# Kernel optimization log

Hardware: AMD Instinct MI355X
Metric: run time of the kernel (lower is better)

The kernel has to match this reference:

```python
import jax, jax.numpy as jnp
import numpy as np

HEADS = 8
DIM_HEAD = 64
QUERY_DIM = 512
CONTEXT_DIM = 768
INNER = HEADS * DIM_HEAD  # 512
SCALE = DIM_HEAD ** -0.5


def setup_inputs() -> dict:
    key = jax.random.key(0)
    ks = jax.random.split(key, 7)
    B, N, M = 4, 2048, 2048
    x = jax.random.normal(ks[0], (B, N, QUERY_DIM), dtype=jnp.float32)
    context = jax.random.normal(ks[1], (B, M, CONTEXT_DIM), dtype=jnp.float32)
    # torch Linear weights: [out_features, in_features], y = x @ W.T
    s = 0.02
    Wq = jax.random.normal(ks[2], (INNER, QUERY_DIM), dtype=jnp.float32) * s
    Wk = jax.random.normal(ks[3], (INNER, CONTEXT_DIM), dtype=jnp.float32) * s
    Wv = jax.random.normal(ks[4], (INNER, CONTEXT_DIM), dtype=jnp.float32) * s
    Wo = jax.random.normal(ks[5], (QUERY_DIM, INNER), dtype=jnp.float32) * s
    bo = jax.random.normal(ks[6], (QUERY_DIM,), dtype=jnp.float32) * s
    return {"x": x, "context": context, "Wq": Wq, "Wk": Wk, "Wv": Wv, "Wo": Wo, "bo": bo}


def reference(x, context, Wq, Wk, Wv, Wo, bo):
    b, n, _ = x.shape
    m = context.shape[1]
    h, d = HEADS, DIM_HEAD
    # Projections (bias=False for q/k/v)
    q = jnp.einsum('bnc,ec->bne', x, Wq)        # [b, n, inner]
    k = jnp.einsum('bmc,ec->bme', context, Wk)  # [b, m, inner]
    v = jnp.einsum('bmc,ec->bme', context, Wv)
    # Split heads
    q = q.reshape(b, n, h, d)
    k = k.reshape(b, m, h, d)
    v = v.reshape(b, m, h, d)
    # Scores in fp32 (original casts q,k to float), scaled by dim_head**-0.5
    sim = jnp.einsum('bihd,bjhd->bhij', q.astype(jnp.float32), k.astype(jnp.float32)) * SCALE
    attn = jax.nn.softmax(sim, axis=-1).astype(v.dtype)
    out = jnp.einsum('bhij,bjhd->bihd', attn, v).reshape(b, n, h * d)
    # Output projection with bias (dropout=0 -> identity)
    return jnp.einsum('bne,oe->bno', out, Wo) + bo
```

## Files before the change

### kernel.cpp

```cpp
#include <hip/hip_runtime.h>
#include <hip/hip_bf16.h>
#include <math.h>


typedef __bf16 bf16x8 __attribute__((ext_vector_type(8)));
typedef __bf16 bf16x4 __attribute__((ext_vector_type(4)));
typedef float f32x4 __attribute__((ext_vector_type(4)));

#define QSCALE 0.18033688011112042f

#if __has_builtin(__builtin_amdgcn_exp2f)
#define EXP2(x) __builtin_amdgcn_exp2f(x)
#else
#define EXP2(x) exp2f(x)
#endif

__device__ __forceinline__ f32x4 mfma32(bf16x8 a, bf16x8 b, f32x4 c) {
  return __builtin_amdgcn_mfma_f32_16x16x32_bf16(a, b, c, 0, 0, 0);
}

__global__ __launch_bounds__(256) void cast_all(
    const float* __restrict__ x, const float* __restrict__ ctx,
    const float* __restrict__ wq, const float* __restrict__ wk,
    const float* __restrict__ wv, const float* __restrict__ wo,
    __bf16* __restrict__ xb, __bf16* __restrict__ cb,
    __bf16* __restrict__ wqb, __bf16* __restrict__ wkb,
    __bf16* __restrict__ wvb, __bf16* __restrict__ wob) {
  const int B0 = 1048576;
  const int B1 = 2621440;
  const int B2 = 2686976;
  const int B3 = 2785280;
  const int B4 = 2883584;
  const int B5 = 2949120;
  for (int i = blockIdx.x * blockDim.x + threadIdx.x; i < B5;
       i += gridDim.x * blockDim.x) {
    const float* s;
    __bf16* d;
    int off;
    if (i < B0)      { s = x;   d = xb;  off = i; }
    else if (i < B1) { s = ctx; d = cb;  off = i - B0; }
    else if (i < B2) { s = wq;  d = wqb; off = i - B1; }
    else if (i < B3) { s = wk;  d = wkb; off = i - B2; }
    else if (i < B4) { s = wv;  d = wvb; off = i - B3; }
    else             { s = wo;  d = wob; off = i - B4; }
    float4 f = ((const float4*)s)[off];
    union { __bf16 b[4]; ushort4 u; } cv;
    cv.b[0] = (__bf16)f.x; cv.b[1] = (__bf16)f.y;
    cv.b[2] = (__bf16)f.z; cv.b[3] = (__bf16)f.w;
    ((ushort4*)d)[off] = cv.u;
  }
}

template <int MODE>
__device__ __forceinline__ void gemm_body(
    const __bf16* __restrict__ A, const __bf16* __restrict__ W,
    __bf16* __restrict__ Cout, int Kd, float scale, int m0, int n0,
    __bf16 (*As)[72], __bf16 (*Bs)[72]) {
  const int t = threadIdx.x;
  const int w = t >> 6;
  const int lane = t & 63;
  const int ln = lane & 15;
  const int qd = lane >> 4;
  const int wm = (w >> 1) * 64;
  const int wn = (w & 1) * 64;

  f32x4 zero4 = {0.f, 0.f, 0.f, 0.f};
  f32x4 acc[4][4];
#pragma unroll
  for (int i = 0; i < 4; ++i)
#pragma unroll
    for (int j = 0; j < 4; ++j) acc[i][j] = zero4;

  const int r0 = t >> 2;
  const int c0 = (t & 3) * 16;
  const __bf16* gA0 = A + (size_t)(m0 + r0) * Kd + c0;
  const __bf16* gA1 = A + (size_t)(m0 + r0 + 64) * Kd + c0;
  const __bf16* gB0 = W + (size_t)(n0 + r0) * Kd + c0;
  const __bf16* gB1 = W + (size_t)(n0 + r0 + 64) * Kd + c0;

  uint4 a00 = *(const uint4*)gA0, a01 = *(const uint4*)(gA0 + 8);
  uint4 a10 = *(const uint4*)gA1, a11 = *(const uint4*)(gA1 + 8);
  uint4 b00 = *(const uint4*)gB0, b01 = *(const uint4*)(gB0 + 8);
  uint4 b10 = *(const uint4*)gB1, b11 = *(const uint4*)(gB1 + 8);

  for (int kc = 0; kc < Kd; kc += 64) {
    __syncthreads();
    *(uint4*)&As[r0][c0] = a00;       *(uint4*)&As[r0][c0 + 8] = a01;
    *(uint4*)&As[r0 + 64][c0] = a10;  *(uint4*)&As[r0 + 64][c0 + 8] = a11;
    *(uint4*)&Bs[r0][c0] = b00;       *(uint4*)&Bs[r0][c0 + 8] = b01;
    *(uint4*)&Bs[r0 + 64][c0] = b10;  *(uint4*)&Bs[r0 + 64][c0 + 8] = b11;
    __syncthreads();
    if (kc + 64 < Kd) {
      a00 = *(const uint4*)(gA0 + kc + 64);
      a01 = *(const uint4*)(gA0 + kc + 72);
      a10 = *(const uint4*)(gA1 + kc + 64);
      a11 = *(const uint4*)(gA1 + kc + 72);
      b00 = *(const uint4*)(gB0 + kc + 64);
      b01 = *(const uint4*)(gB0 + kc + 72);
      b10 = *(const uint4*)(gB1 + kc + 64);
      b11 = *(const uint4*)(gB1 + kc + 72);
    }
#pragma unroll
    for (int kst = 0; kst < 2; ++kst) {
      bf16x8 af[4], bfr[4];
#pragma unroll
      for (int i = 0; i < 4; ++i) {
        af[i] = *(const bf16x8*)&As[wm + i * 16 + ln][kst * 32 + qd * 8];
        bfr[i] = *(const bf16x8*)&Bs[wn + i * 16 + ln][kst * 32 + qd * 8];
      }
#pragma unroll
      for (int i = 0; i < 4; ++i)
#pragma unroll
        for (int j = 0; j < 4; ++j) {
          if (MODE == 1)
            acc[i][j] = mfma32(af[i], bfr[j], acc[i][j]);
          else
            acc[i][j] = mfma32(bfr[j], af[i], acc[i][j]);
        }
    }
  }

#pragma unroll
  for (int i = 0; i < 4; ++i)
#pragma unroll
    for (int j = 0; j < 4; ++j) {
      if (MODE == 0) {
        const int gm = m0 + wm + i * 16 + ln;
        const int gn0 = n0 + wn + j * 16 + qd * 4;
        const int bb = gm >> 11, tok = gm & 2047;
        const int hh = gn0 >> 6, dd0 = gn0 & 63;
        bf16x4 v;
#pragma unroll
        for (int rg = 0; rg < 4; ++rg) v[rg] = (__bf16)(acc[i][j][rg] * scale);
        *(bf16x4*)(Cout + (((size_t)bb * 8 + hh) * 2048 + tok) * 64 + dd0) = v;
      } else {
        const int gm0 = m0 + wm + i * 16 + qd * 4;
        const int gn = n0 + wn + j * 16 + ln;
        const int bb = gm0 >> 11, tok0 = gm0 & 2047;
        const int hh = gn >> 6, dd = gn & 63;
        bf16x4 v;
#pragma unroll
        for (int rg = 0; rg < 4; ++rg) v[rg] = (__bf16)acc[i][j][rg];
        *(bf16x4*)(Cout + (((size_t)bb * 8 + hh) * 64 + dd) * 2048 + tok0) = v;
      }
    }
}

__global__ __launch_bounds__(256, 3) void proj_qkv(
    const __bf16* __restrict__ xb, const __bf16* __restrict__ cb,
    const __bf16* __restrict__ Wq, const __bf16* __restrict__ Wk,
    const __bf16* __restrict__ Wv, __bf16* __restrict__ Qw,
    __bf16* __restrict__ Kw, __bf16* __restrict__ Vtw) {
  __shared__ __align__(16) __bf16 As[128][72];
  __shared__ __align__(16) __bf16 Bs[128][72];
  const int m0 = blockIdx.x * 128;
  const int job = blockIdx.y >> 2;
  const int n0 = (blockIdx.y & 3) * 128;
  if (job == 0)
    gemm_body<0>(xb, Wq, Qw, 512, QSCALE, m0, n0, As, Bs);
  else if (job == 1)
    gemm_body<0>(cb, Wk, Kw, 768, 1.0f, m0, n0, As, Bs);
  else
    gemm_body<1>(cb, Wv, Vtw, 768, 1.0f, m0, n0, As, Bs);
}

__global__ __launch_bounds__(256) void gemm_out(
    const __bf16* __restrict__ O0, const __bf16* __restrict__ O1,
    const float* __restrict__ lbuf,
    const __bf16* __restrict__ B,
    float* __restrict__ C, const float* __restrict__ bias) {
  const int m0 = blockIdx.x * 64;
  const int n0 = blockIdx.y * 128;
  const int t = threadIdx.x;
  const int w = t >> 6;
  const int lane = t & 63;
  const int ln = lane & 15;
  const int qd = lane >> 4;
  const int wm = (w >> 1) * 32;
  const int wn = (w & 1) * 64;

  __shared__ __align__(16) __bf16 As[64][72];
  __shared__ __align__(16) __bf16 Bs[128][72];

  f32x4 zero4 = {0.f, 0.f, 0.f, 0.f};
  f32x4 acc[2][4];
#pragma unroll
  for (int i = 0; i < 2; ++i)
#pragma unroll
    for (int j = 0; j < 4; ++j) acc[i][j] = zero4;

  const int r0 = t >> 2;
  const int c0 = (t & 3) * 16;
  const int gm_s = m0 + r0;
  const int bidx = gm_s >> 11, tok_s = gm_s & 2047;
  const size_t aoff = (size_t)gm_s * 512 + c0;
  const __bf16* gB0 = B + (size_t)(n0 + r0) * 512 + c0;
  const __bf16* gB1 = B + (size_t)(n0 + r0 + 64) * 512 + c0;

  float inv[8];
#pragma unroll
  for (int hh = 0; hh < 8; ++hh) {
    const float l0 = lbuf[((size_t)bidx * 8 + hh) * 2048 + tok_s];
    const float l1 = lbuf[65536 + ((size_t)bidx * 8 + hh) * 2048 + tok_s];
    inv[hh] = 1.0f / (l0 + l1);
  }

  uint4 o00 = *(const uint4*)(O0 + aoff), o01 = *(const uint4*)(O0 + aoff + 8);
  uint4 o10 = *(const uint4*)(O1 + aoff), o11 = *(const uint4*)(O1 + aoff + 8);
  uint4 b00 = *(const uint4*)gB0, b01 = *(const uint4*)(gB0 + 8);
  uint4 b10 = *(const uint4*)gB1, b11 = *(const uint4*)(gB1 + 8);

  for (int kc = 0; kc < 512; kc += 64) {
    const float iv = inv[kc >> 6];
    union { bf16x8 v; uint4 u; } u0, u1, r0v, r1v;
    u0.u = o00; u1.u = o10;
#pragma unroll
    for (int e = 0; e < 8; ++e)
      r0v.v[e] = (__bf16)(((float)u0.v[e] + (float)u1.v[e]) * iv);
    u0.u = o01; u1.u = o11;
#pragma unroll
    for (int e = 0; e < 8; ++e)
      r1v.v[e] = (__bf16)(((float)u0.v[e] + (float)u1.v[e]) * iv);
    __syncthreads();
    *(uint4*)&As[r0][c0] = r0v.u;
    *(uint4*)&As[r0][c0 + 8] = r1v.u;
    *(uint4*)&Bs[r0][c0] = b00;       *(uint4*)&Bs[r0][c0 + 8] = b01;
    *(uint4*)&Bs[r0 + 64][c0] = b10;  *(uint4*)&Bs[r0 + 64][c0 + 8] = b11;
    __syncthreads();
    if (kc + 64 < 512) {
      o00 = *(const uint4*)(O0 + aoff + kc + 64);
      o01 = *(const uint4*)(O0 + aoff + kc + 72);
      o10 = *(const uint4*)(O1 + aoff + kc + 64);
      o11 = *(const uint4*)(O1 + aoff + kc + 72);
      b00 = *(const uint4*)(gB0 + kc + 64);
      b01 = *(const uint4*)(gB0 + kc + 72);
      b10 = *(const uint4*)(gB1 + kc + 64);
      b11 = *(const uint4*)(gB1 + kc + 72);
    }
#pragma unroll
    for (int kst = 0; kst < 2; ++kst) {
      bf16x8 af[2], bfr[4];
#pragma unroll
      for (int i = 0; i < 2; ++i)
        af[i] = *(const bf16x8*)&As[wm + i * 16 + ln][kst * 32 + qd * 8];
#pragma unroll
      for (int j = 0; j < 4; ++j)
        bfr[j] = *(const bf16x8*)&Bs[wn + j * 16 + ln][kst * 32 + qd * 8];
#pragma unroll
      for (int i = 0; i < 2; ++i)
#pragma unroll
        for (int j = 0; j < 4; ++j)
          acc[i][j] = mfma32(bfr[j], af[i], acc[i][j]);
    }
  }

#pragma unroll
  for (int i = 0; i < 2; ++i)
#pragma unroll
    for (int j = 0; j < 4; ++j) {
      const int gm = m0 + wm + i * 16 + ln;
      const int gn0 = n0 + wn + j * 16 + qd * 4;
      f32x4 bi = *(const f32x4*)&bias[gn0];
      f32x4 v = acc[i][j] + bi;
      *(f32x4*)&C[(size_t)gm * 512 + gn0] = v;
    }
}

__global__ __launch_bounds__(256, 2) void attn_kernel(
    const __bf16* __restrict__ Q,
    const __bf16* __restrict__ K,
    const __bf16* __restrict__ Vt,
    __bf16* __restrict__ Oh,
    float* __restrict__ lbuf) {
  const int S = 2048;
  const int qt = blockIdx.x;
  const int bh = blockIdx.y;
  const int sp = blockIdx.z;
  const int b = bh >> 3, h = bh & 7;
  const int t = threadIdx.x;
  const int w = t >> 6;
  const int lane = t & 63;
  const int ln = lane & 15;
  const int qd = lane >> 4;

  __shared__ __align__(16) __bf16 Ks[2][128][72];
  __shared__ __align__(16) __bf16 Vs[2][64][136];

  bf16x8 bq[4][2];
  {
    const __bf16* qb =
        Q + ((size_t)bh * S + qt * 256 + w * 64 + ln) * 64 + qd * 8;
#pragma unroll
    for (int mt = 0; mt < 4; ++mt)
#pragma unroll
      for (int kst = 0; kst < 2; ++kst)
        bq[mt][kst] = *(const bf16x8*)(qb + mt * 1024 + kst * 32);
  }

  f32x4 zero4 = {0.f, 0.f, 0.f, 0.f};
  f32x4 o[4][4];
  f32x4 o_l[4];
#pragma unroll
  for (int mt = 0; mt < 4; ++mt) {
#pragma unroll
    for (int i = 0; i < 4; ++i) o[mt][i] = zero4;
    o_l[mt] = zero4;
  }
  bf16x8 ones8;
  {
    union { unsigned short u[8]; bf16x8 v; } U;
#pragma unroll
    for (int e = 0; e < 8; ++e) U.u[e] = 0x3F80;
    ones8 = U.v;
  }

  const int kr = t >> 2, kc0 = (t & 3) * 16;
  const int krow =
      (kr & ~31) | ((kr & 4) << 2) | (((kr >> 3) & 3) << 2) | (kr & 3);
  const int vd = t >> 3, vtok0 = (t & 7) * 16;
  const int kt0 = sp * 8;

  const __bf16* gK0 = K + ((size_t)bh * S + kt0 * 128 + kr) * 64 + kc0;
  const __bf16* gK1 = gK0 + 4096;
  const __bf16* gV0 = Vt + ((size_t)bh * 64 + vd) * S + kt0 * 128 + vtok0;
  const __bf16* gV1 = gV0 + 65536;

  {
    uint4 k00 = ((const uint4*)gK0)[0], k01 = ((const uint4*)gK0)[1];
    uint4 k10 = ((const uint4*)gK1)[0], k11 = ((const uint4*)gK1)[1];
    uint4 v00 = ((const uint4*)gV0)[0], v01 = ((const uint4*)gV0)[1];
    uint4 v10 = ((const uint4*)gV1)[0], v11 = ((const uint4*)gV1)[1];
    uint4* dK0 = (uint4*)&Ks[0][krow][kc0];      dK0[0] = k00; dK0[1] = k01;
    uint4* dK1 = (uint4*)&Ks[0][krow + 64][kc0]; dK1[0] = k10; dK1[1] = k11;
    uint4* dV0 = (uint4*)&Vs[0][vd][vtok0];      dV0[0] = v00; dV0[1] = v01;
    uint4* dV1 = (uint4*)&Vs[0][vd + 32][vtok0]; dV1[0] = v10; dV1[1] = v11;
  }
  uint4 pk00 = ((const uint4*)(gK0 + 8192))[0];
  uint4 pk01 = ((const uint4*)(gK0 + 8192))[1];
  uint4 pk10 = ((const uint4*)(gK1 + 8192))[0];
  uint4 pk11 = ((const uint4*)(gK1 + 8192))[1];
  uint4 pv00 = ((const uint4*)(gV0 + 128))[0];
  uint4 pv01 = ((const uint4*)(gV0 + 128))[1];
  uint4 pv10 = ((const uint4*)(gV1 + 128))[0];
  uint4 pv11 = ((const uint4*)(gV1 + 128))[1];
  __syncthreads();

  int p = 0;
  for (int it = 0; it < 8; ++it) {
    if (it + 1 < 8) {
      uint4* dK0 = (uint4*)&Ks[p ^ 1][krow][kc0];
      dK0[0] = pk00; dK0[1] = pk01;
      uint4* dK1 = (uint4*)&Ks[p ^ 1][krow + 64][kc0];
      dK1[0] = pk10; dK1[1] = pk11;
      uint4* dV0 = (uint4*)&Vs[p ^ 1][vd][vtok0];
      dV0[0] = pv00; dV0[1] = pv01;
      uint4* dV1 = (uint4*)&Vs[p ^ 1][vd + 32][vtok0];
      dV1[0] = pv10; dV1[1] = pv11;
      if (it + 2 < 8) {
        const __bf16* nK0 = gK0 + (size_t)(it + 2) * 8192;
        const __bf16* nK1 = gK1 + (size_t)(it + 2) * 8192;
        const __bf16* nV0 = gV0 + (size_t)(it + 2) * 128;
        const __bf16* nV1 = gV1 + (size_t)(it + 2) * 128;
        pk00 = ((const uint4*)nK0)[0]; pk01 = ((const uint4*)nK0)[1];
        pk10 = ((const uint4*)nK1)[0]; pk11 = ((const uint4*)nK1)[1];
        pv00 = ((const uint4*)nV0)[0]; pv01 = ((const uint4*)nV0)[1];
        pv10 = ((const uint4*)nV1)[0]; pv11 = ((const uint4*)nV1)[1];
      }
    }

    const __bf16 (*Ksp)[72] = Ks[p];
    const __bf16 (*Vsp)[136] = Vs[p];

#pragma unroll
    for (int c = 0; c < 4; ++c) {
      bf16x8 ak[2][2];
#pragma unroll
      for (int e = 0; e < 2; ++e)
#pragma unroll
        for (int kst = 0; kst < 2; ++kst)
          ak[e][kst] =
              *(const bf16x8*)&Ksp[(c * 2 + e) * 16 + ln][kst * 32 + qd * 8];
      bf16x8 av[4];
#pragma unroll
      for (int i = 0; i < 4; ++i)
        av[i] = *(const bf16x8*)&Vsp[i * 16 + ln][c * 32 + qd * 8];

      f32x4 s[4][2];
      __builtin_amdgcn_s_setprio(1);
#pragma unroll
      for (int mt = 0; mt < 4; ++mt) {
        s[mt][0] = zero4;
        s[mt][1] = zero4;
#pragma unroll
        for (int kst = 0; kst < 2; ++kst) {
          s[mt][0] = mfma32(ak[0][kst], bq[mt][kst], s[mt][0]);
          s[mt][1] = mfma32(ak[1][kst], bq[mt][kst], s[mt][1]);
        }
      }
      __builtin_amdgcn_s_setprio(0);

      bf16x8 p2[4];
#pragma unroll
      for (int mt = 0; mt < 4; ++mt) {
#pragma unroll
        for (int rg = 0; rg < 4; ++rg) {
          p2[mt][rg] = (__bf16)EXP2(s[mt][0][rg]);
          p2[mt][rg + 4] = (__bf16)EXP2(s[mt][1][rg]);
        }
      }

      __builtin_amdgcn_s_setprio(1);
#pragma unroll
      for (int mt = 0; mt < 4; ++mt) {
        o_l[mt] = mfma32(ones8, p2[mt], o_l[mt]);
#pragma unroll
        for (int i = 0; i < 4; ++i)
          o[mt][i] = mfma32(av[i], p2[mt], o[mt][i]);
      }
      __builtin_amdgcn_s_setprio(0);
    }

    __syncthreads();
    p ^= 1;
  }

  __bf16* Osp = Oh + (size_t)sp * 8192 * 512;
#pragma unroll
  for (int mt = 0; mt < 4; ++mt) {
    const int tok = qt * 256 + w * 64 + mt * 16 + ln;
    if (qd == 0) lbuf[((size_t)sp * 32 + bh) * 2048 + tok] = o_l[mt][0];
#pragma unroll
    for (int i = 0; i < 4; ++i) {
      bf16x4 v;
#pragma unroll
      for (int rg = 0; rg < 4; ++rg) v[rg] = (__bf16)o[mt][i][rg];
      const int col = h * 64 + i * 16 + qd * 4;
      *(bf16x4*)&Osp[((size_t)b * S + tok) * 512 + col] = v;
    }
  }
}

extern "C" void kernel_launch(void* const* d_in, const int* in_sizes, int n_in,
                              void* d_out, int out_size, void* d_ws,
                              size_t ws_size, hipStream_t stream) {
  const float* x = (const float*)d_in[0];
  const float* ctx = (const float*)d_in[1];
  const float* Wq = (const float*)d_in[2];
  const float* Wk = (const float*)d_in[3];
  const float* Wv = (const float*)d_in[4];
  const float* Wo = (const float*)d_in[5];
  const float* bo = (const float*)d_in[6];

  char* p = (char*)d_ws;
  __bf16* xb = (__bf16*)p;   p += (size_t)8192 * 512 * 2;
  __bf16* cb = (__bf16*)p;   p += (size_t)8192 * 768 * 2;
  __bf16* wqb = (__bf16*)p;  p += (size_t)512 * 512 * 2;
  __bf16* wkb = (__bf16*)p;  p += (size_t)512 * 768 * 2;
  __bf16* wvb = (__bf16*)p;  p += (size_t)512 * 768 * 2;
  __bf16* wob = (__bf16*)p;  p += (size_t)512 * 512 * 2;
  __bf16* Qw = (__bf16*)p;   p += (size_t)8192 * 512 * 2;
  __bf16* Kw = (__bf16*)p;   p += (size_t)8192 * 512 * 2;
  __bf16* Vtw = (__bf16*)p;  p += (size_t)8192 * 512 * 2;
  __bf16* Oh = (__bf16*)p;   p += (size_t)2 * 8192 * 512 * 2;
  float* lbuf = (float*)p;   p += (size_t)2 * 32 * 2048 * 4;

  cast_all<<<2880, 256, 0, stream>>>(x, ctx, Wq, Wk, Wv, Wo, xb, cb, wqb, wkb,
                                     wvb, wob);

  dim3 gp(64, 12);
  proj_qkv<<<gp, 256, 0, stream>>>(xb, cb, wqb, wkb, wvb, Qw, Kw, Vtw);

  dim3 ga(8, 32, 2);
  attn_kernel<<<ga, 256, 0, stream>>>(Qw, Kw, Vtw, Oh, lbuf);

  dim3 go(128, 4);
  gemm_out<<<go, 256, 0, stream>>>(Oh, Oh + (size_t)8192 * 512, lbuf, wob,
                                   (float*)d_out, bo);
}
```

Baseline: 173.4 us.

## Split attention KV range four ways with smaller 64-token tiles

The attention kernel now splits the key/value sequence into four partitions instead of two and processes 64-token KV tiles rather than 128, which shrinks shared memory and raises the occupancy hint to 4 blocks per CU. The grid doubles to expose more parallel blocks. The output GEMM now sums four partial outputs and four row-sum buffers before normalising. This adds partial-output write and read traffic and a larger workspace in exchange for more parallelism in attention. The unseen part of the attention kernel (softmax and partial stores) is assumed to match the new tile size and split index.

```diff
diff --git a/kernel.cpp b/kernel.cpp
--- a/kernel.cpp
+++ b/kernel.cpp
@@ -165,10 +165,11 @@
 }
 
 __global__ __launch_bounds__(256) void gemm_out(
-    const __bf16* __restrict__ O0, const __bf16* __restrict__ O1,
+    const __bf16* __restrict__ Oh,
     const float* __restrict__ lbuf,
     const __bf16* __restrict__ B,
     float* __restrict__ C, const float* __restrict__ bias) {
+  const size_t SLAB = (size_t)8192 * 512;
   const int m0 = blockIdx.x * 64;
   const int n0 = blockIdx.y * 128;
   const int t = threadIdx.x;
@@ -200,27 +201,35 @@
   float inv[8];
 #pragma unroll
   for (int hh = 0; hh < 8; ++hh) {
-    const float l0 = lbuf[((size_t)bidx * 8 + hh) * 2048 + tok_s];
-    const float l1 = lbuf[65536 + ((size_t)bidx * 8 + hh) * 2048 + tok_s];
-    inv[hh] = 1.0f / (l0 + l1);
-  }
-
-  uint4 o00 = *(const uint4*)(O0 + aoff), o01 = *(const uint4*)(O0 + aoff + 8);
-  uint4 o10 = *(const uint4*)(O1 + aoff), o11 = *(const uint4*)(O1 + aoff + 8);
+    float l = 0.f;
+#pragma unroll
+    for (int k = 0; k < 4; ++k)
+      l += lbuf[(size_t)k * 65536 + ((size_t)bidx * 8 + hh) * 2048 + tok_s];
+    inv[hh] = 1.0f / l;
+  }
+
+  uint4 oA[4], oB[4];
+#pragma unroll
+  for (int k = 0; k < 4; ++k) {
+    oA[k] = *(const uint4*)(Oh + (size_t)k * SLAB + aoff);
+    oB[k] = *(const uint4*)(Oh + (size_t)k * SLAB + aoff + 8);
+  }
   uint4 b00 = *(const uint4*)gB0, b01 = *(const uint4*)(gB0 + 8);
   uint4 b10 = *(const uint4*)gB1, b11 = *(const uint4*)(gB1 + 8);
 
   for (int kc = 0; kc < 512; kc += 64) {
     const float iv = inv[kc >> 6];
-    union { bf16x8 v; uint4 u; } u0, u1, r0v, r1v;
-    u0.u = o00; u1.u = o10;
+    union { bf16x8 v; uint4 u; } u0, u1, u2, u3, r0v, r1v;
+    u0.u = oA[0]; u1.u = oA[1]; u2.u = oA[2]; u3.u = oA[3];
 #pragma unroll
     for (int e = 0; e < 8; ++e)
-      r0v.v[e] = (__bf16)(((float)u0.v[e] + (float)u1.v[e]) * iv);
-    u0.u = o01; u1.u = o11;
+      r0v.v[e] = (__bf16)((((float)u0.v[e] + (float)u1.v[e]) +
+                           ((float)u2.v[e] + (float)u3.v[e])) * iv);
+    u0.u = oB[0]; u1.u = oB[1]; u2.u = oB[2]; u3.u = oB[3];
 #pragma unroll
     for (int e = 0; e < 8; ++e)
-      r1v.v[e] = (__bf16)(((float)u0.v[e] + (float)u1.v[e]) * iv);
+      r1v.v[e] = (__bf16)((((float)u0.v[e] + (float)u1.v[e]) +
+                           ((float)u2.v[e] + (float)u3.v[e])) * iv);
     __syncthreads();
     *(uint4*)&As[r0][c0] = r0v.u;
     *(uint4*)&As[r0][c0 + 8] = r1v.u;
@@ -228,10 +237,11 @@
     *(uint4*)&Bs[r0 + 64][c0] = b10;  *(uint4*)&Bs[r0 + 64][c0 + 8] = b11;
     __syncthreads();
     if (kc + 64 < 512) {
-      o00 = *(const uint4*)(O0 + aoff + kc + 64);
-      o01 = *(const uint4*)(O0 + aoff + kc + 72);
-      o10 = *(const uint4*)(O1 + aoff + kc + 64);
-      o11 = *(const uint4*)(O1 + aoff + kc + 72);
+#pragma unroll
+      for (int k = 0; k < 4; ++k) {
+        oA[k] = *(const uint4*)(Oh + (size_t)k * SLAB + aoff + kc + 64);
+        oB[k] = *(const uint4*)(Oh + (size_t)k * SLAB + aoff + kc + 72);
+      }
       b00 = *(const uint4*)(gB0 + kc + 64);
       b01 = *(const uint4*)(gB0 + kc + 72);
       b10 = *(const uint4*)(gB1 + kc + 64);
@@ -266,7 +276,7 @@
     }
 }
 
-__global__ __launch_bounds__(256, 2) void attn_kernel(
+__global__ __launch_bounds__(256, 4) void attn_kernel(
     const __bf16* __restrict__ Q,
     const __bf16* __restrict__ K,
     const __bf16* __restrict__ Vt,
@@ -283,8 +293,8 @@
   const int ln = lane & 15;
   const int qd = lane >> 4;
 
-  __shared__ __align__(16) __bf16 Ks[2][128][72];
-  __shared__ __align__(16) __bf16 Vs[2][64][136];
+  __shared__ __align__(16) __bf16 Ks[2][64][72];
+  __shared__ __align__(16) __bf16 Vs[2][64][72];
 
   bf16x8 bq[4][2];
   {
@@ -317,62 +327,45 @@
   const int kr = t >> 2, kc0 = (t & 3) * 16;
   const int krow =
       (kr & ~31) | ((kr & 4) << 2) | (((kr >> 3) & 3) << 2) | (kr & 3);
-  const int vd = t >> 3, vtok0 = (t & 7) * 16;
   const int kt0 = sp * 8;
 
-  const __bf16* gK0 = K + ((size_t)bh * S + kt0 * 128 + kr) * 64 + kc0;
-  const __bf16* gK1 = gK0 + 4096;
-  const __bf16* gV0 = Vt + ((size_t)bh * 64 + vd) * S + kt0 * 128 + vtok0;
-  const __bf16* gV1 = gV0 + 65536;
+  const __bf16* gK0 = K + ((size_t)bh * S + kt0 * 64 + kr) * 64 + kc0;
+  const __bf16* gV0 = Vt + ((size_t)bh * 64 + kr) * S + kt0 * 64 + kc0;
 
   {
-    uint4 k00 = ((const uint4*)gK0)[0], k01 = ((const uint4*)gK0)[1];
-    uint4 k10 = ((const uint4*)gK1)[0], k11 = ((const uint4*)gK1)[1];
-    uint4 v00 = ((const uint4*)gV0)[0], v01 = ((const uint4*)gV0)[1];
-    uint4 v10 = ((const uint4*)gV1)[0], v11 = ((const uint4*)gV1)[1];
-    uint4* dK0 = (uint4*)&Ks[0][krow][kc0];      dK0[0] = k00; dK0[1] = k01;
-    uint4* dK1 = (uint4*)&Ks[0][krow + 64][kc0]; dK1[0] = k10; dK1[1] = k11;
-    uint4* dV0 = (uint4*)&Vs[0][vd][vtok0];      dV0[0] = v00; dV0[1] = v01;
-    uint4* dV1 = (uint4*)&Vs[0][vd + 32][vtok0]; dV1[0] = v10; dV1[1] = v11;
-  }
-  uint4 pk00 = ((const uint4*)(gK0 + 8192))[0];
-  uint4 pk01 = ((const uint4*)(gK0 + 8192))[1];
-  uint4 pk10 = ((const uint4*)(gK1 + 8192))[0];
-  uint4 pk11 = ((const uint4*)(gK1 + 8192))[1];
-  uint4 pv00 = ((const uint4*)(gV0 + 128))[0];
-  uint4 pv01 = ((const uint4*)(gV0 + 128))[1];
-  uint4 pv10 = ((const uint4*)(gV1 + 128))[0];
-  uint4 pv11 = ((const uint4*)(gV1 + 128))[1];
+    uint4 k0 = ((const uint4*)gK0)[0], k1 = ((const uint4*)gK0)[1];
+    uint4 v0 = ((const uint4*)gV0)[0], v1 = ((const uint4*)gV0)[1];
+    uint4* dK = (uint4*)&Ks[0][krow][kc0];
+    dK[0] = k0; dK[1] = k1;
+    uint4* dV = (uint4*)&Vs[0][kr][kc0];
+    dV[0] = v0; dV[1] = v1;
+  }
+  uint4 pk0 = ((const uint4*)(gK0 + 4096))[0];
+  uint4 pk1 = ((const uint4*)(gK0 + 4096))[1];
+  uint4 pv0 = ((const uint4*)(gV0 + 64))[0];
+  uint4 pv1 = ((const uint4*)(gV0 + 64))[1];
   __syncthreads();
 
   int p = 0;
   for (int it = 0; it < 8; ++it) {
     if (it + 1 < 8) {
-      uint4* dK0 = (uint4*)&Ks[p ^ 1][krow][kc0];
-      dK0[0] = pk00; dK0[1] = pk01;
-      uint4* dK1 = (uint4*)&Ks[p ^ 1][krow + 64][kc0];
-      dK1[0] = pk10; dK1[1] = pk11;
-      uint4* dV0 = (uint4*)&Vs[p ^ 1][vd][vtok0];
-      dV0[0] = pv00; dV0[1] = pv01;
-      uint4* dV1 = (uint4*)&Vs[p ^ 1][vd + 32][vtok0];
-      dV1[0] = pv10; dV1[1] = pv11;
+      uint4* dK = (uint4*)&Ks[p ^ 1][krow][kc0];
+      dK[0] = pk0; dK[1] = pk1;
+      uint4* dV = (uint4*)&Vs[p ^ 1][kr][kc0];
+      dV[0] = pv0; dV[1] = pv1;
       if (it + 2 < 8) {
-        const __bf16* nK0 = gK0 + (size_t)(it + 2) * 8192;
-        const __bf16* nK1 = gK1 + (size_t)(it + 2) * 8192;
-        const __bf16* nV0 = gV0 + (size_t)(it + 2) * 128;
-        const __bf16* nV1 = gV1 + (size_t)(it + 2) * 128;
-        pk00 = ((const uint4*)nK0)[0]; pk01 = ((const uint4*)nK0)[1];
-        pk10 = ((const uint4*)nK1)[0]; pk11 = ((const uint4*)nK1)[1];
-        pv00 = ((const uint4*)nV0)[0]; pv01 = ((const uint4*)nV0)[1];
-        pv10 = ((const uint4*)nV1)[0]; pv11 = ((const uint4*)nV1)[1];
+        const __bf16* nK = gK0 + (size_t)(it + 2) * 4096;
+        const __bf16* nV = gV0 + (size_t)(it + 2) * 64;
+        pk0 = ((const uint4*)nK)[0]; pk1 = ((const uint4*)nK)[1];
+        pv0 = ((const uint4*)nV)[0]; pv1 = ((const uint4*)nV)[1];
       }
     }
 
     const __bf16 (*Ksp)[72] = Ks[p];
-    const __bf16 (*Vsp)[136] = Vs[p];
-
-#pragma unroll
-    for (int c = 0; c < 4; ++c) {
+    const __bf16 (*Vsp)[72] = Vs[p];
+
+#pragma unroll
+    for (int c = 0; c < 2; ++c) {
       bf16x8 ak[2][2];
 #pragma unroll
       for (int e = 0; e < 2; ++e)
@@ -461,8 +454,8 @@
   __bf16* Qw = (__bf16*)p;   p += (size_t)8192 * 512 * 2;
   __bf16* Kw = (__bf16*)p;   p += (size_t)8192 * 512 * 2;
   __bf16* Vtw = (__bf16*)p;  p += (size_t)8192 * 512 * 2;
-  __bf16* Oh = (__bf16*)p;   p += (size_t)2 * 8192 * 512 * 2;
-  float* lbuf = (float*)p;   p += (size_t)2 * 32 * 2048 * 4;
+  __bf16* Oh = (__bf16*)p;   p += (size_t)4 * 8192 * 512 * 2;
+  float* lbuf = (float*)p;   p += (size_t)4 * 32 * 2048 * 4;
 
   cast_all<<<2880, 256, 0, stream>>>(x, ctx, Wq, Wk, Wv, Wo, xb, cb, wqb, wkb,
                                      wvb, wob);
@@ -470,10 +463,9 @@
   dim3 gp(64, 12);
   proj_qkv<<<gp, 256, 0, stream>>>(xb, cb, wqb, wkb, wvb, Qw, Kw, Vtw);
 
-  dim3 ga(8, 32, 2);
+  dim3 ga(8, 32, 4);
   attn_kernel<<<ga, 256, 0, stream>>>(Qw, Kw, Vtw, Oh, lbuf);
 
   dim3 go(128, 4);
-  gemm_out<<<go, 256, 0, stream>>>(Oh, Oh + (size_t)8192 * 512, lbuf, wob,
-                                   (float*)d_out, bo);
-}
+  gemm_out<<<go, 256, 0, stream>>>(Oh, lbuf, wob, (float*)d_out, bo);
+}
```

Result: slower. 475.1 us (+174.0%).
